# Kernel optimization log

Hardware: AMD Instinct MI355X
Metric: run time of the kernel (lower is better)

The kernel has to match this reference:

```python
import jax, jax.numpy as jnp
import numpy as np

B, S, D = 4, 2048, 768
H = 12
HD = D // H  # 64


def setup_inputs() -> dict:
    key = jax.random.key(0)
    k1, k2, k3 = jax.random.split(key, 3)
    x = jax.random.normal(k1, (B, S, D), dtype=jnp.float32)
    w_qkv = jax.random.normal(k2, (D, 3 * D), dtype=jnp.float32) * (1.0 / np.sqrt(D))
    b_qkv = jnp.zeros((3 * D,), dtype=jnp.float32)
    w_proj = jax.random.normal(k3, (D, D), dtype=jnp.float32) * (1.0 / np.sqrt(D))
    b_proj = jnp.zeros((D,), dtype=jnp.float32)
    return {"x": x, "w_qkv": w_qkv, "b_qkv": b_qkv, "w_proj": w_proj, "b_proj": b_proj}


def reference(x, w_qkv, b_qkv, w_proj, b_proj):
    b, s, d = x.shape
    qkv = x @ w_qkv + b_qkv                      # [B,S,3D]
    q, k, v = jnp.split(qkv, 3, axis=-1)
    # [B,S,D] -> [B,H,S,HD]
    q = q.reshape(b, s, H, HD).transpose(0, 2, 1, 3)
    k = k.reshape(b, s, H, HD).transpose(0, 2, 1, 3)
    v = v.reshape(b, s, H, HD).transpose(0, 2, 1, 3)
    scores = jnp.einsum("bhqd,bhkd->bhqk", q, k) / jnp.sqrt(jnp.float32(HD))
    causal = jnp.tril(jnp.ones((s, s), dtype=bool))
    scores = jnp.where(causal[None, None, :, :], scores, jnp.float32(-jnp.inf))
    attn = jax.nn.softmax(scores, axis=-1)       # dropout p=0.0 -> identity
    out = jnp.einsum("bhqk,bhkd->bhqd", attn, v)  # [B,H,S,HD]
    out = out.transpose(0, 2, 1, 3).reshape(b, s, d)
    return out @ w_proj + b_proj
```

## Files before the change

kernel.cpp:

```cpp
#include <hip/hip_runtime.h>
#include <hip/hip_bf16.h>

typedef __hip_bfloat16 bf16;
typedef __bf16 bf16x8 __attribute__((ext_vector_type(8)));
typedef float f32x4 __attribute__((ext_vector_type(4)));

#define MFMA(a, b, c) __builtin_amdgcn_mfma_f32_16x16x32_bf16(a, b, c, 0, 0, 0)
#define EXP2F(x) __builtin_exp2f(x)

constexpr int Bn = 4, Sn = 2048, Dn = 768, Hn = 12;
constexpr int N3 = 3 * Dn;
constexpr int Mrows = Bn * Sn;

constexpr size_t XB_OFF    = 0;
constexpr size_t WQKV_OFF  = 12582912;
constexpr size_t WPROJ_OFF = 16121856;
constexpr size_t Q_OFF     = 17301504;
constexpr size_t K_OFF     = 29884416;
constexpr size_t VT_OFF    = 42467328;
constexpr size_t O_OFF     = 55050240;

#define QSCALE 0.1803368801111243f

__device__ __forceinline__ void gload16(const void* g, void* l) {
  __builtin_amdgcn_global_load_lds((__attribute__((address_space(1))) void*)g,
                                   (__attribute__((address_space(3))) void*)l,
                                   16, 0, 0);
}

__device__ __forceinline__ unsigned int cvt_pk_bf16(float lo, float hi) {
  unsigned int r;
  asm("v_cvt_pk_bf16_f32 %0, %1, %2" : "=v"(r) : "v"(lo), "v"(hi));
  return r;
}
__device__ __forceinline__ unsigned short f2bfu(float f) {
  return (unsigned short)(cvt_pk_bf16(f, f) & 0xffffu);
}

__global__ __launch_bounds__(256) void cvt_x_kernel(const float* __restrict__ in,
                                                    bf16* __restrict__ out, int n4) {
  int i = blockIdx.x * 256 + threadIdx.x;
  if (i >= n4) return;
  float4 f = reinterpret_cast<const float4*>(in)[i];
  uint2 o;
  o.x = cvt_pk_bf16(f.x, f.y);
  o.y = cvt_pk_bf16(f.z, f.w);
  reinterpret_cast<uint2*>(out)[i] = o;
}

__global__ __launch_bounds__(256) void transpose_cvt(const float* __restrict__ in,
                                                     bf16* __restrict__ out, int K, int N) {
  __shared__ float tile[32][33];
  int n0 = blockIdx.x * 32, k0 = blockIdx.y * 32;
  int tx = threadIdx.x & 31, ty = threadIdx.x >> 5;
  for (int r = ty; r < 32; r += 8)
    tile[r][tx] = in[(size_t)(k0 + r) * N + n0 + tx];
  __syncthreads();
  for (int r = ty; r < 32; r += 8)
    out[(size_t)(n0 + r) * K + k0 + tx] = __float2bfloat16(tile[tx][r]);
}

__global__ __launch_bounds__(256) void gemm_qkv(const bf16* __restrict__ A,
                                                const bf16* __restrict__ BT,
                                                const float* __restrict__ bias,
                                                bf16* __restrict__ Qo,
                                                bf16* __restrict__ Ko,
                                                bf16* __restrict__ Vt) {
  __shared__ __align__(16) bf16 As[2][128 * 32];
  __shared__ __align__(16) bf16 Bs[2][128 * 32];
  const int tid = threadIdx.x;
  const int m0 = blockIdx.x * 128, n0 = blockIdx.y * 128;
  const int w = tid >> 6, lane = tid & 63;
  const int wr = w >> 1, wc = w & 1;
  const int lr = lane & 15, lg = lane >> 4;

  f32x4 acc[4][4] = {};

  auto stage = [&](int k0, int sb) {
    for (int r = 0; r < 2; ++r) {
      int c = tid + r * 256;
      int row = c >> 2, ch = c & 3;
      int gch = ch ^ ((row >> 1) & 3);
      gload16(A + (size_t)(m0 + row) * Dn + k0 + gch * 8, &As[sb][c * 8]);
      gload16(BT + (size_t)(n0 + row) * Dn + k0 + gch * 8, &Bs[sb][c * 8]);
    }
  };

  stage(0, 0);
  __syncthreads();

  const int sw = (lr >> 1) & 3;
  const int aoff = (wr * 64 + lr) * 32 + ((lg ^ sw) << 3);
  const int boff = (wc * 64 + lr) * 32 + ((lg ^ sw) << 3);
  int buf = 0;

  for (int kt = 0; kt < 24; ++kt) {
    if (kt < 23) stage((kt + 1) * 32, buf ^ 1);
    bf16x8 af[4], bfr[4];
    for (int mi = 0; mi < 4; ++mi)
      af[mi] = *reinterpret_cast<const bf16x8*>(&As[buf][aoff + mi * 512]);
    for (int ni = 0; ni < 4; ++ni)
      bfr[ni] = *reinterpret_cast<const bf16x8*>(&Bs[buf][boff + ni * 512]);
    for (int mi = 0; mi < 4; ++mi)
      for (int ni = 0; ni < 4; ++ni)
        acc[mi][ni] = MFMA(af[mi], bfr[ni], acc[mi][ni]);
    __syncthreads();
    buf ^= 1;
  }

  for (int ni = 0; ni < 4; ++ni) {
    const int col = n0 + wc * 64 + ni * 16 + lr;
    const float bv = bias[col];
    const int seg = (col >= Dn) + (col >= 2 * Dn);
    const int d = col - seg * Dn;
    const int h = d >> 6, hd = d & 63;
    for (int mi = 0; mi < 4; ++mi) {
      f32x4 v = acc[mi][ni];
      const int row0 = m0 + wr * 64 + mi * 16 + lg * 4;
      const int b = row0 >> 11, s0 = row0 & 2047;
      const size_t bh = (size_t)(b * Hn + h);
      if (seg == 2) {
        uint2 pk;
        pk.x = cvt_pk_bf16(v[0] + bv, v[1] + bv);
        pk.y = cvt_pk_bf16(v[2] + bv, v[3] + bv);
        *reinterpret_cast<uint2*>(&Vt[(bh * 64 + hd) * Sn + s0]) = pk;
      } else if (seg == 0) {
        for (int r = 0; r < 4; ++r)
          Qo[(bh * Sn + s0 + r) * 64 + hd] = __float2bfloat16((v[r] + bv) * QSCALE);
      } else {
        for (int r = 0; r < 4; ++r)
          Ko[(bh * Sn + s0 + r) * 64 + hd] = __float2bfloat16(v[r] + bv);
      }
    }
  }
}

__global__ __launch_bounds__(256) void attn_fwd(const bf16* __restrict__ Q,
                                                const bf16* __restrict__ K,
                                                const bf16* __restrict__ Vt,
                                                bf16* __restrict__ O) {
  __shared__ __align__(16) bf16 Ks[2][64 * 64];
  __shared__ __align__(16) bf16 Vs[2][64 * 64];
  __shared__ __align__(16) bf16 Ps[4][16 * 64];
  const int tid = threadIdx.x, w = tid >> 6, lane = tid & 63;
  const int lr = lane & 15, lg = lane >> 4;
  const int bid = blockIdx.x;
  const int qt = 31 - (bid / 48);
  const int bh = bid % 48;
  const int q0 = qt * 64;
  const size_t base = (size_t)bh * Sn * 64;
  const int wrow = q0 + w * 16;

  bf16x8 qf[2];
  for (int kk = 0; kk < 2; ++kk)
    qf[kk] = *reinterpret_cast<const bf16x8*>(
        Q + base + (size_t)(wrow + lr) * 64 + kk * 32 + lg * 8);

  f32x4 o[4] = {};
  float mrow = -1e30f, lrow = 0.f;

  const int nt = qt + 1;

  auto stage = [&](int t, int sb) {
    for (int rr = 0; rr < 2; ++rr) {
      int c = tid + rr * 256;
      int row = c >> 3, cp = c & 7;
      int sc = cp ^ (row & 7);
      gload16(K + base + (size_t)t * 4096 + row * 64 + sc * 8, &Ks[sb][c * 8]);
      gload16(Vt + base + (size_t)row * Sn + t * 64 + sc * 8, &Vs[sb][c * 8]);
    }
  };

  stage(0, 0);
  __syncthreads();
  int buf = 0;
  for (int t = 0; t < nt; ++t) {
    if (t + 1 < nt) stage(t + 1, buf ^ 1);

    f32x4 sf[4];
    for (int ni = 0; ni < 4; ++ni) {
      const int krow = ni * 16 + lr;
      bf16x8 kf0 = *reinterpret_cast<const bf16x8*>(&Ks[buf][krow * 64 + (lg ^ (lr & 7)) * 8]);
      bf16x8 kf1 = *reinterpret_cast<const bf16x8*>(&Ks[buf][krow * 64 + ((4 + lg) ^ (lr & 7)) * 8]);
      f32x4 z = {};
      z = MFMA(kf0, qf[0], z);
      z = MFMA(kf1, qf[1], z);
      sf[ni] = z;
    }
    if (t == nt - 1) {
      const int qg = wrow + lr;
      for (int ni = 0; ni < 4; ++ni)
        for (int r = 0; r < 4; ++r) {
          int kg = t * 64 + ni * 16 + lg * 4 + r;
          if (kg > qg) sf[ni][r] = -1e30f;
        }
    }
    float ma = fmaxf(fmaxf(sf[0][0], sf[0][1]), fmaxf(sf[0][2], sf[0][3]));
    float mb = fmaxf(fmaxf(sf[1][0], sf[1][1]), fmaxf(sf[1][2], sf[1][3]));
    float mc = fmaxf(fmaxf(sf[2][0], sf[2][1]), fmaxf(sf[2][2], sf[2][3]));
    float md = fmaxf(fmaxf(sf[3][0], sf[3][1]), fmaxf(sf[3][2], sf[3][3]));
    float vmax = fmaxf(fmaxf(ma, mb), fmaxf(mc, md));
    vmax = fmaxf(vmax, __shfl_xor(vmax, 16));
    vmax = fmaxf(vmax, __shfl_xor(vmax, 32));
    if (!__all(vmax - mrow <= 8.0f)) {
      const float mnew = fmaxf(mrow, vmax);
      const float alpha = EXP2F(mrow - mnew);
      lrow *= alpha;
      for (int di = 0; di < 4; ++di) {
        f32x4 ov = o[di];
        ov[0] *= alpha; ov[1] *= alpha; ov[2] *= alpha; ov[3] *= alpha;
        o[di] = ov;
      }
      mrow = mnew;
    }
    float ps = 0.f;
    for (int ni = 0; ni < 4; ++ni) {
      f32x4 z = sf[ni];
      z[0] = EXP2F(z[0] - mrow);
      z[1] = EXP2F(z[1] - mrow);
      z[2] = EXP2F(z[2] - mrow);
      z[3] = EXP2F(z[3] - mrow);
      sf[ni] = z;
      ps += (z[0] + z[1]) + (z[2] + z[3]);
    }
    ps += __shfl_xor(ps, 16);
    ps += __shfl_xor(ps, 32);
    lrow += ps;
    for (int ni = 0; ni < 4; ++ni) {
      const int chunk = ni * 2 + (lg >> 1);
      const int eoff = lr * 64 + ((chunk ^ (lr & 7)) << 3) + ((lg & 1) << 2);
      uint2 pk;
      pk.x = cvt_pk_bf16(sf[ni][0], sf[ni][1]);
      pk.y = cvt_pk_bf16(sf[ni][2], sf[ni][3]);
      *reinterpret_cast<uint2*>(&Ps[w][eoff]) = pk;
    }
    asm volatile("s_waitcnt lgkmcnt(0)" ::: "memory");
    __builtin_amdgcn_sched_barrier(0);
    for (int kk = 0; kk < 2; ++kk) {
      bf16x8 pf = *reinterpret_cast<const bf16x8*>(
          &Ps[w][lr * 64 + (((kk * 4 + lg) ^ (lr & 7)) << 3)]);
      for (int di = 0; di < 4; ++di) {
        bf16x8 vf = *reinterpret_cast<const bf16x8*>(
            &Vs[buf][(di * 16 + lr) * 64 + (((kk * 4 + lg) ^ (lr & 7)) << 3)]);
        o[di] = MFMA(vf, pf, o[di]);
      }
    }
    __syncthreads();
    buf ^= 1;
  }

  const int b = bh / Hn, h = bh % Hn;
  const float inv = 1.0f / lrow;
  const size_t rowbase = ((size_t)b * Sn + wrow + lr) * Dn + h * 64;
  for (int di = 0; di < 4; ++di) {
    f32x4 ov = o[di];
    uint2 pk;
    pk.x = cvt_pk_bf16(ov[0] * inv, ov[1] * inv);
    pk.y = cvt_pk_bf16(ov[2] * inv, ov[3] * inv);
    *reinterpret_cast<uint2*>(&O[rowbase + di * 16 + lg * 4]) = pk;
  }
}

__global__ __launch_bounds__(256) void gemm_proj(const bf16* __restrict__ A,
                                                 const bf16* __restrict__ BT,
                                                 const float* __restrict__ bias,
                                                 float* __restrict__ out) {
  __shared__ __align__(16) bf16 As[2][128 * 32];
  __shared__ __align__(16) bf16 Bs[2][128 * 32];
  const int tid = threadIdx.x;
  const int m0 = blockIdx.x * 128, n0 = blockIdx.y * 128;
  const int w = tid >> 6, lane = tid & 63;
  const int wr = w >> 1, wc = w & 1;
  const int lr = lane & 15, lg = lane >> 4;

  f32x4 acc[4][4] = {};

  auto stage = [&](int k0, int sb) {
    for (int r = 0; r < 2; ++r) {
      int c = tid + r * 256;
      int row = c >> 2, ch = c & 3;
      int gch = ch ^ ((row >> 1) & 3);
      gload16(A + (size_t)(m0 + row) * Dn + k0 + gch * 8, &As[sb][c * 8]);
      gload16(BT + (size_t)(n0 + row) * Dn + k0 + gch * 8, &Bs[sb][c * 8]);
    }
  };

  stage(0, 0);
  __syncthreads();

  const int sw = (lr >> 1) & 3;
  const int aoff = (wr * 64 + lr) * 32 + ((lg ^ sw) << 3);
  const int boff = (wc * 64 + lr) * 32 + ((lg ^ sw) << 3);
  int buf = 0;

  for (int kt = 0; kt < 24; ++kt) {
    if (kt < 23) stage((kt + 1) * 32, buf ^ 1);
    bf16x8 af[4], bfr[4];
    for (int mi = 0; mi < 4; ++mi)
      af[mi] = *reinterpret_cast<const bf16x8*>(&As[buf][aoff + mi * 512]);
    for (int ni = 0; ni < 4; ++ni)
      bfr[ni] = *reinterpret_cast<const bf16x8*>(&Bs[buf][boff + ni * 512]);
    for (int mi = 0; mi < 4; ++mi)
      for (int ni = 0; ni < 4; ++ni)
        acc[mi][ni] = MFMA(af[mi], bfr[ni], acc[mi][ni]);
    __syncthreads();
    buf ^= 1;
  }

  for (int ni = 0; ni < 4; ++ni) {
    const int col = n0 + wc * 64 + ni * 16 + lr;
    const float bv = bias[col];
    for (int mi = 0; mi < 4; ++mi) {
      f32x4 v = acc[mi][ni];
      for (int r = 0; r < 4; ++r) {
        const int row = m0 + wr * 64 + mi * 16 + lg * 4 + r;
        out[(size_t)row * Dn + col] = v[r] + bv;
      }
    }
  }
}

extern "C" void kernel_launch(void* const* d_in, const int* in_sizes, int n_in,
                              void* d_out, int out_size, void* d_ws, size_t ws_size,
                              hipStream_t stream) {
  const float* x      = (const float*)d_in[0];
  const float* w_qkv  = (const float*)d_in[1];
  const float* b_qkv  = (const float*)d_in[2];
  const float* w_proj = (const float*)d_in[3];
  const float* b_proj = (const float*)d_in[4];
  float* out = (float*)d_out;

  char* ws = (char*)d_ws;
  bf16* xb     = (bf16*)(ws + XB_OFF);
  bf16* wqkvT  = (bf16*)(ws + WQKV_OFF);
  bf16* wprojT = (bf16*)(ws + WPROJ_OFF);
  bf16* Qb     = (bf16*)(ws + Q_OFF);
  bf16* Kb     = (bf16*)(ws + K_OFF);
  bf16* Vtb    = (bf16*)(ws + VT_OFF);
  bf16* Ob     = (bf16*)(ws + O_OFF);

  cvt_x_kernel<<<(Mrows * Dn / 4 + 255) / 256, 256, 0, stream>>>(x, xb, Mrows * Dn / 4);
  transpose_cvt<<<dim3(N3 / 32, Dn / 32), 256, 0, stream>>>(w_qkv, wqkvT, Dn, N3);
  transpose_cvt<<<dim3(Dn / 32, Dn / 32), 256, 0, stream>>>(w_proj, wprojT, Dn, Dn);
  gemm_qkv<<<dim3(Mrows / 128, N3 / 128), 256, 0, stream>>>(xb, wqkvT, b_qkv, Qb, Kb, Vtb);
  attn_fwd<<<32 * 48, 256, 0, stream>>>(Qb, Kb, Vtb, Ob);
  gemm_proj<<<dim3(Mrows / 128, Dn / 128), 256, 0, stream>>>(Ob, wprojT, b_proj, out);
}
```

Baseline: 153.8 us.

## Enlarge attention query tile to 128 rows with two row groups per wave

The attention kernel now processes 128 query rows per block, each wave handling 32 rows as two 16-row MFMA groups. Every K/V tile staged in LDS is reused across twice as many queries, halving the number of K/V loads and the grid size. Waves skip tiles lying entirely above their causal diagonal, and MFMA sections are wrapped in s_setprio hints. The cost is more registers per wave, half as many blocks, and idle waves on the diagonal tiles, which may reduce occupancy and load balance.

```diff
diff --git a/kernel.cpp b/kernel.cpp
--- a/kernel.cpp
+++ b/kernel.cpp
@@ -32,9 +32,6 @@
   unsigned int r;
   asm("v_cvt_pk_bf16_f32 %0, %1, %2" : "=v"(r) : "v"(lo), "v"(hi));
   return r;
-}
-__device__ __forceinline__ unsigned short f2bfu(float f) {
-  return (unsigned short)(cvt_pk_bf16(f, f) & 0xffffu);
 }
 
 __global__ __launch_bounds__(256) void cvt_x_kernel(const float* __restrict__ in,
@@ -141,25 +138,26 @@
                                                 bf16* __restrict__ O) {
   __shared__ __align__(16) bf16 Ks[2][64 * 64];
   __shared__ __align__(16) bf16 Vs[2][64 * 64];
-  __shared__ __align__(16) bf16 Ps[4][16 * 64];
+  __shared__ __align__(16) bf16 Ps[4][32 * 64];
   const int tid = threadIdx.x, w = tid >> 6, lane = tid & 63;
   const int lr = lane & 15, lg = lane >> 4;
   const int bid = blockIdx.x;
-  const int qt = 31 - (bid / 48);
+  const int qt = 15 - (bid / 48);
   const int bh = bid % 48;
-  const int q0 = qt * 64;
+  const int q0 = qt * 128;
   const size_t base = (size_t)bh * Sn * 64;
-  const int wrow = q0 + w * 16;
-
-  bf16x8 qf[2];
-  for (int kk = 0; kk < 2; ++kk)
-    qf[kk] = *reinterpret_cast<const bf16x8*>(
-        Q + base + (size_t)(wrow + lr) * 64 + kk * 32 + lg * 8);
-
-  f32x4 o[4] = {};
-  float mrow = -1e30f, lrow = 0.f;
-
-  const int nt = qt + 1;
+  const int wrow = q0 + w * 32;
+
+  bf16x8 qf[2][2];
+  for (int mi = 0; mi < 2; ++mi)
+    for (int kk = 0; kk < 2; ++kk)
+      qf[mi][kk] = *reinterpret_cast<const bf16x8*>(
+          Q + base + (size_t)(wrow + mi * 16 + lr) * 64 + kk * 32 + lg * 8);
+
+  f32x4 o[2][4] = {};
+  float mrow[2] = {-1e30f, -1e30f}, lrow[2] = {0.f, 0.f};
+
+  const int nt = 2 * qt + 2;
 
   auto stage = [&](int t, int sb) {
     for (int rr = 0; rr < 2; ++rr) {
@@ -177,87 +175,102 @@
   for (int t = 0; t < nt; ++t) {
     if (t + 1 < nt) stage(t + 1, buf ^ 1);
 
-    f32x4 sf[4];
-    for (int ni = 0; ni < 4; ++ni) {
-      const int krow = ni * 16 + lr;
-      bf16x8 kf0 = *reinterpret_cast<const bf16x8*>(&Ks[buf][krow * 64 + (lg ^ (lr & 7)) * 8]);
-      bf16x8 kf1 = *reinterpret_cast<const bf16x8*>(&Ks[buf][krow * 64 + ((4 + lg) ^ (lr & 7)) * 8]);
-      f32x4 z = {};
-      z = MFMA(kf0, qf[0], z);
-      z = MFMA(kf1, qf[1], z);
-      sf[ni] = z;
-    }
-    if (t == nt - 1) {
-      const int qg = wrow + lr;
-      for (int ni = 0; ni < 4; ++ni)
-        for (int r = 0; r < 4; ++r) {
-          int kg = t * 64 + ni * 16 + lg * 4 + r;
-          if (kg > qg) sf[ni][r] = -1e30f;
-        }
-    }
-    float ma = fmaxf(fmaxf(sf[0][0], sf[0][1]), fmaxf(sf[0][2], sf[0][3]));
-    float mb = fmaxf(fmaxf(sf[1][0], sf[1][1]), fmaxf(sf[1][2], sf[1][3]));
-    float mc = fmaxf(fmaxf(sf[2][0], sf[2][1]), fmaxf(sf[2][2], sf[2][3]));
-    float md = fmaxf(fmaxf(sf[3][0], sf[3][1]), fmaxf(sf[3][2], sf[3][3]));
-    float vmax = fmaxf(fmaxf(ma, mb), fmaxf(mc, md));
-    vmax = fmaxf(vmax, __shfl_xor(vmax, 16));
-    vmax = fmaxf(vmax, __shfl_xor(vmax, 32));
-    if (!__all(vmax - mrow <= 8.0f)) {
-      const float mnew = fmaxf(mrow, vmax);
-      const float alpha = EXP2F(mrow - mnew);
-      lrow *= alpha;
-      for (int di = 0; di < 4; ++di) {
-        f32x4 ov = o[di];
-        ov[0] *= alpha; ov[1] *= alpha; ov[2] *= alpha; ov[3] *= alpha;
-        o[di] = ov;
-      }
-      mrow = mnew;
-    }
-    float ps = 0.f;
-    for (int ni = 0; ni < 4; ++ni) {
-      f32x4 z = sf[ni];
-      z[0] = EXP2F(z[0] - mrow);
-      z[1] = EXP2F(z[1] - mrow);
-      z[2] = EXP2F(z[2] - mrow);
-      z[3] = EXP2F(z[3] - mrow);
-      sf[ni] = z;
-      ps += (z[0] + z[1]) + (z[2] + z[3]);
-    }
-    ps += __shfl_xor(ps, 16);
-    ps += __shfl_xor(ps, 32);
-    lrow += ps;
-    for (int ni = 0; ni < 4; ++ni) {
-      const int chunk = ni * 2 + (lg >> 1);
-      const int eoff = lr * 64 + ((chunk ^ (lr & 7)) << 3) + ((lg & 1) << 2);
-      uint2 pk;
-      pk.x = cvt_pk_bf16(sf[ni][0], sf[ni][1]);
-      pk.y = cvt_pk_bf16(sf[ni][2], sf[ni][3]);
-      *reinterpret_cast<uint2*>(&Ps[w][eoff]) = pk;
-    }
-    asm volatile("s_waitcnt lgkmcnt(0)" ::: "memory");
-    __builtin_amdgcn_sched_barrier(0);
-    for (int kk = 0; kk < 2; ++kk) {
-      bf16x8 pf = *reinterpret_cast<const bf16x8*>(
-          &Ps[w][lr * 64 + (((kk * 4 + lg) ^ (lr & 7)) << 3)]);
-      for (int di = 0; di < 4; ++di) {
-        bf16x8 vf = *reinterpret_cast<const bf16x8*>(
-            &Vs[buf][(di * 16 + lr) * 64 + (((kk * 4 + lg) ^ (lr & 7)) << 3)]);
-        o[di] = MFMA(vf, pf, o[di]);
-      }
+    if (t * 64 <= wrow + 31) {
+      f32x4 sf[2][4];
+      __builtin_amdgcn_s_setprio(1);
+      for (int ni = 0; ni < 4; ++ni) {
+        const int krow = ni * 16 + lr;
+        bf16x8 kf0 = *reinterpret_cast<const bf16x8*>(&Ks[buf][krow * 64 + (lg ^ (lr & 7)) * 8]);
+        bf16x8 kf1 = *reinterpret_cast<const bf16x8*>(&Ks[buf][krow * 64 + ((4 + lg) ^ (lr & 7)) * 8]);
+        for (int mi = 0; mi < 2; ++mi) {
+          f32x4 z = {};
+          z = MFMA(kf0, qf[mi][0], z);
+          z = MFMA(kf1, qf[mi][1], z);
+          sf[mi][ni] = z;
+        }
+      }
+      __builtin_amdgcn_s_setprio(0);
+      if (t * 64 + 63 > wrow) {
+        for (int mi = 0; mi < 2; ++mi) {
+          const int qg = wrow + mi * 16 + lr;
+          for (int ni = 0; ni < 4; ++ni)
+            for (int r = 0; r < 4; ++r) {
+              int kg = t * 64 + ni * 16 + lg * 4 + r;
+              if (kg > qg) sf[mi][ni][r] = -1e30f;
+            }
+        }
+      }
+      for (int mi = 0; mi < 2; ++mi) {
+        float ma = fmaxf(fmaxf(sf[mi][0][0], sf[mi][0][1]), fmaxf(sf[mi][0][2], sf[mi][0][3]));
+        float mb = fmaxf(fmaxf(sf[mi][1][0], sf[mi][1][1]), fmaxf(sf[mi][1][2], sf[mi][1][3]));
+        float mc = fmaxf(fmaxf(sf[mi][2][0], sf[mi][2][1]), fmaxf(sf[mi][2][2], sf[mi][2][3]));
+        float md = fmaxf(fmaxf(sf[mi][3][0], sf[mi][3][1]), fmaxf(sf[mi][3][2], sf[mi][3][3]));
+        float vmax = fmaxf(fmaxf(ma, mb), fmaxf(mc, md));
+        vmax = fmaxf(vmax, __shfl_xor(vmax, 16));
+        vmax = fmaxf(vmax, __shfl_xor(vmax, 32));
+        if (!__all(vmax - mrow[mi] <= 8.0f)) {
+          const float mnew = fmaxf(mrow[mi], vmax);
+          const float alpha = EXP2F(mrow[mi] - mnew);
+          lrow[mi] *= alpha;
+          for (int di = 0; di < 4; ++di) {
+            f32x4 ov = o[mi][di];
+            ov[0] *= alpha; ov[1] *= alpha; ov[2] *= alpha; ov[3] *= alpha;
+            o[mi][di] = ov;
+          }
+          mrow[mi] = mnew;
+        }
+        float ps = 0.f;
+        for (int ni = 0; ni < 4; ++ni) {
+          f32x4 z = sf[mi][ni];
+          z[0] = EXP2F(z[0] - mrow[mi]);
+          z[1] = EXP2F(z[1] - mrow[mi]);
+          z[2] = EXP2F(z[2] - mrow[mi]);
+          z[3] = EXP2F(z[3] - mrow[mi]);
+          sf[mi][ni] = z;
+          ps += (z[0] + z[1]) + (z[2] + z[3]);
+        }
+        ps += __shfl_xor(ps, 16);
+        ps += __shfl_xor(ps, 32);
+        lrow[mi] += ps;
+        for (int ni = 0; ni < 4; ++ni) {
+          const int chunk = ni * 2 + (lg >> 1);
+          const int eoff = (mi * 16 + lr) * 64 + ((chunk ^ (lr & 7)) << 3) + ((lg & 1) << 2);
+          uint2 pk;
+          pk.x = cvt_pk_bf16(sf[mi][ni][0], sf[mi][ni][1]);
+          pk.y = cvt_pk_bf16(sf[mi][ni][2], sf[mi][ni][3]);
+          *reinterpret_cast<uint2*>(&Ps[w][eoff]) = pk;
+        }
+      }
+      asm volatile("s_waitcnt lgkmcnt(0)" ::: "memory");
+      __builtin_amdgcn_sched_barrier(0);
+      __builtin_amdgcn_s_setprio(1);
+      for (int kk = 0; kk < 2; ++kk) {
+        const int psw = ((kk * 4 + lg) ^ (lr & 7)) << 3;
+        bf16x8 pf0 = *reinterpret_cast<const bf16x8*>(&Ps[w][lr * 64 + psw]);
+        bf16x8 pf1 = *reinterpret_cast<const bf16x8*>(&Ps[w][(16 + lr) * 64 + psw]);
+        for (int di = 0; di < 4; ++di) {
+          bf16x8 vf = *reinterpret_cast<const bf16x8*>(&Vs[buf][(di * 16 + lr) * 64 + psw]);
+          o[0][di] = MFMA(vf, pf0, o[0][di]);
+          o[1][di] = MFMA(vf, pf1, o[1][di]);
+        }
+      }
+      __builtin_amdgcn_s_setprio(0);
     }
     __syncthreads();
     buf ^= 1;
   }
 
   const int b = bh / Hn, h = bh % Hn;
-  const float inv = 1.0f / lrow;
-  const size_t rowbase = ((size_t)b * Sn + wrow + lr) * Dn + h * 64;
-  for (int di = 0; di < 4; ++di) {
-    f32x4 ov = o[di];
-    uint2 pk;
-    pk.x = cvt_pk_bf16(ov[0] * inv, ov[1] * inv);
-    pk.y = cvt_pk_bf16(ov[2] * inv, ov[3] * inv);
-    *reinterpret_cast<uint2*>(&O[rowbase + di * 16 + lg * 4]) = pk;
+  for (int mi = 0; mi < 2; ++mi) {
+    const float inv = 1.0f / lrow[mi];
+    const size_t rowbase = ((size_t)b * Sn + wrow + mi * 16 + lr) * Dn + h * 64;
+    for (int di = 0; di < 4; ++di) {
+      f32x4 ov = o[mi][di];
+      uint2 pk;
+      pk.x = cvt_pk_bf16(ov[0] * inv, ov[1] * inv);
+      pk.y = cvt_pk_bf16(ov[2] * inv, ov[3] * inv);
+      *reinterpret_cast<uint2*>(&O[rowbase + di * 16 + lg * 4]) = pk;
+    }
   }
 }
 
@@ -343,6 +356,6 @@
   transpose_cvt<<<dim3(N3 / 32, Dn / 32), 256, 0, stream>>>(w_qkv, wqkvT, Dn, N3);
   transpose_cvt<<<dim3(Dn / 32, Dn / 32), 256, 0, stream>>>(w_proj, wprojT, Dn, Dn);
   gemm_qkv<<<dim3(Mrows / 128, N3 / 128), 256, 0, stream>>>(xb, wqkvT, b_qkv, Qb, Kb, Vtb);
-  attn_fwd<<<32 * 48, 256, 0, stream>>>(Qb, Kb, Vtb, Ob);
+  attn_fwd<<<16 * 48, 256, 0, stream>>>(Qb, Kb, Vtb, Ob);
   gemm_proj<<<dim3(Mrows / 128, Dn / 128), 256, 0, stream>>>(Ob, wprojT, b_proj, out);
 }
```

Result: no change. 156.7 us (+1.9%).
